# Optimization experiments

Hardware: AMD Instinct MI355X
Metric: run time of the kernel (lower is better)

The kernel has to match this reference:

```python
import jax, jax.numpy as jnp
import numpy as np

N_PTS = 100000
C_IN, C_OUT, K = 16, 32, 3
B, D, H, W = 2, 32, 128, 128


def setup_inputs() -> dict:
    key = jax.random.key(0)
    kf, kw, kb, kz, ky, kx = jax.random.split(key, 6)
    features = jax.random.normal(kf, (N_PTS, C_IN), dtype=jnp.float32)
    coords = jnp.stack([
        jax.random.randint(kb, (N_PTS,), 0, B),
        jax.random.randint(kz, (N_PTS,), 0, D),
        jax.random.randint(ky, (N_PTS,), 0, H),
        jax.random.randint(kx, (N_PTS,), 0, W),
    ], axis=1).astype(jnp.int32)
    weight = jax.random.normal(kw, (K ** 3, C_IN, C_OUT), dtype=jnp.float32) * 0.01
    bias = jnp.zeros((C_OUT,), dtype=jnp.float32)
    return {"features": features, "coords": coords, "weight": weight, "bias": bias,
            "batch_size": B, "d_sp": D, "h_sp": H, "w_sp": W}


def reference(features, coords, weight, bias, batch_size, d_sp, h_sp, w_sp):
    # Scatter sparse voxel features into dense grid (B, C_in, D, H, W).
    n, c_in = features.shape
    c_out = weight.shape[2]
    k = K
    b, z, y, x = coords[:, 0], coords[:, 1], coords[:, 2], coords[:, 3]
    dense = jnp.zeros((batch_size, c_in, d_sp, h_sp, w_sp), dtype=features.dtype)
    dense = dense.at[b, :, z, y, x].set(features)  # (N,) advanced idx -> rows of (N, C_in)
    # Conv3d: torch copies weight.view(C_out, C_in, k, k, k) -> OIDHW kernel.
    kernel = weight.reshape(c_out, c_in, k, k, k)
    out = jax.lax.conv_general_dilated(
        dense, kernel,
        window_strides=(1, 1, 1),
        padding=[(1, 1), (1, 1), (1, 1)],
        dimension_numbers=("NCDHW", "OIDHW", "NCDHW"))
    out = jax.nn.relu(out + bias[None, :, None, None, None])
    # Dense equivalent of the torch nonzero-gather (which has data-dependent
    # shape): return the full dense activated grid (B, C_out, D, H, W).
    return out
```

## Files before the change

kernel.cpp:

```cpp
#include <hip/hip_runtime.h>

#define CIN   16
#define COUT  32
#define BATCH 2
#define DSP   32
#define HSP   128
#define WSP   128
#define NVOX  (BATCH*DSP*HSP*WSP)

#define DP (DSP+2)
#define HP (HSP+2)
#define WP (WSP+2)
#define NVOXP (BATCH*DP*HP*WP)
#define NDCH  (NVOXP*2)

#define TZ 2
#define TY 4
#define TX 16
#define NTW 8
#define PZ 4
#define PYY 6
#define PXX 18
#define PROW (PYY*PXX)
#define PVOX (PZ*PROW)
#define NCHUNK (2*PVOX)
#define SLICE  (NCHUNK/4)
#define NPAIR 14
#define NWEL  (NPAIR*2*64*8)
#define NWREP ((NWEL + 255)/256)
#define NBLK  1024

typedef __bf16 bf16x8 __attribute__((ext_vector_type(8)));
typedef float  f32x4  __attribute__((ext_vector_type(4)));

__device__ __forceinline__ void load_lds16(const void* g, void* l) {
    __builtin_amdgcn_global_load_lds(
        (const __attribute__((address_space(1))) unsigned*)g,
        (__attribute__((address_space(3))) unsigned*)l, 16, 0, 0);
}

__global__ void k_prep(const int4* __restrict__ coords, int n, int nbDedup,
                       int* __restrict__ map,
                       const float* __restrict__ w, __bf16* __restrict__ wpack) {
    int bb = blockIdx.x;
    if (bb < nbDedup) {
        int p = bb * 256 + threadIdx.x;
        if (p >= n) return;
        int4 c = coords[p];
        int vox = ((c.x*DSP + c.y)*HSP + c.z)*WSP + c.w;
        atomicMax(&map[vox], p);
    } else {
        int i = (bb - nbDedup) * 256 + threadIdx.x;
        if (i >= NWEL) return;
        int j = i & 7, l = (i>>3) & 63, h = (i>>9) & 1, p = i >> 10;
        int tap = 2*p + ((l>>4)>>1);
        int co  = h*16 + (l & 15);
        int ci  = ((l>>4)&1)*8 + j;
        float v = (tap < 27) ? w[(co*CIN + ci)*27 + tap] : 0.0f;
        wpack[i] = (__bf16)v;
    }
}

__global__ void k_fill(const int* __restrict__ map, const float* __restrict__ feat,
                       __bf16* __restrict__ dense) {
    int c = blockIdx.x * 256 + threadIdx.x;
    if (c >= NDCH) return;
    int v = c >> 1, h = c & 1;
    int bb = v / (DP*HP*WP);
    int r  = v - bb*(DP*HP*WP);
    int zp = r / (HP*WP);  r -= zp*(HP*WP);
    int yp = r / WP;
    int xp = r - yp*WP;
    bf16x8 val = { (__bf16)0.f,(__bf16)0.f,(__bf16)0.f,(__bf16)0.f,
                   (__bf16)0.f,(__bf16)0.f,(__bf16)0.f,(__bf16)0.f };
    if ((unsigned)(zp-1) < DSP && (unsigned)(yp-1) < HSP && (unsigned)(xp-1) < WSP) {
        int vox = ((bb*DSP + (zp-1))*HSP + (yp-1))*WSP + (xp-1);
        int p = map[vox];
        if (p >= 0) {
            const float4* fp = (const float4*)(feat + (size_t)p*CIN) + h*2;
            float4 f0 = fp[0], f1 = fp[1];
            val = bf16x8{ (__bf16)f0.x,(__bf16)f0.y,(__bf16)f0.z,(__bf16)f0.w,
                          (__bf16)f1.x,(__bf16)f1.y,(__bf16)f1.z,(__bf16)f1.w };
        }
    }
    *(bf16x8*)(dense + (size_t)v*CIN + h*8) = val;
}

__device__ __forceinline__ void stage_tile(const __bf16* __restrict__ gb,
                                           ushort* lbase, int wave, int lane) {
    #pragma unroll
    for (int it = 0; it < 4; ++it) {
        int rel = it*64 + lane;
        if (rel < SLICE) {
            int j = wave*SLICE + rel;
            int h = (j >= PVOX) ? 1 : 0;
            int v = j - h*PVOX;
            int pz = v / PROW;
            int rm = v - pz*PROW;
            int py = rm / PXX;
            int px = rm - py*PXX;
            load_lds16(gb + ((size_t)(pz*HP*WP + py*WP + px))*CIN + h*8,
                       (void*)(lbase + (size_t)(wave*SLICE + it*64)*8));
        }
    }
}

__global__ __launch_bounds__(256, 3) void k_conv(
    const __bf16* __restrict__ dense, const __bf16* __restrict__ wpack,
    const float* __restrict__ bias, float* __restrict__ out)
{
    __shared__ __align__(16) ushort patch[2][NCHUNK*8];

    int bid = blockIdx.x;
    int bs  = (bid & 7) * (NBLK/8) + (bid >> 3);
    int tyi = bs & 31, tzi = (bs >> 5) & 15, b = bs >> 9;
    int z0 = tzi*TZ, y0 = tyi*TY;

    int tid  = threadIdx.x;
    int lane = tid & 63, wave = tid >> 6;
    int lx16  = lane & 15;
    int lhalf = (lane >> 4) & 1;
    int ltp   = (lane >> 4) >> 1;
    int lq    = lane >> 4;
    int zw    = wave >> 1;
    int yb    = (wave & 1) * 2;

    bf16x8 wf[NPAIR][2];
    #pragma unroll
    for (int p = 0; p < NPAIR; ++p)
        #pragma unroll
        for (int h = 0; h < 2; ++h)
            wf[p][h] = *(const bf16x8*)(wpack + (size_t)((p*2 + h)*64 + lane)*8);

    int voff[NPAIR];
    #pragma unroll
    for (int p = 0; p < NPAIR; ++p) {
        int tap = 2*p + ltp; if (tap > 26) tap = 26;
        int kd = tap/9, kh = (tap/3)%3, kw = tap%3;
        voff[p] = (kd*PYY + kh)*PXX + kw;
    }
    float bv0 = bias[lx16], bv1 = bias[16 + lx16];

    const __bf16* gbase = dense + ((((size_t)b*DP + z0)*HP + y0)*WP)*CIN;

    stage_tile(gbase, patch[0], wave, lane);

    #pragma unroll 1
    for (int t = 0; t < NTW; ++t) {
        if (t < NTW-1)
            stage_tile(gbase + (size_t)(t+1)*TX*CIN, patch[(t&1)^1], wave, lane);
        if (t == 0 || t == NTW-1)
            asm volatile("s_waitcnt vmcnt(4)\ns_barrier" ::: "memory");
        else
            asm volatile("s_waitcnt vmcnt(8)\ns_barrier" ::: "memory");
        __builtin_amdgcn_sched_barrier(0);

        f32x4 acc[2][2];
        acc[0][0] = (f32x4){0.f,0.f,0.f,0.f}; acc[0][1] = (f32x4){0.f,0.f,0.f,0.f};
        acc[1][0] = (f32x4){0.f,0.f,0.f,0.f}; acc[1][1] = (f32x4){0.f,0.f,0.f,0.f};
        const ushort* pb = patch[t&1] +
            ((size_t)lhalf*PVOX + (zw*PYY + yb)*PXX + lx16)*8;
        __builtin_amdgcn_s_setprio(1);
        #pragma unroll
        for (int p = 0; p < NPAIR; ++p) {
            const ushort* pa = pb + (size_t)voff[p]*8;
            #pragma unroll
            for (int gi = 0; gi < 2; ++gi) {
                bf16x8 a = *(const bf16x8*)(pa + gi*(PXX*8));
                acc[gi][0] = __builtin_amdgcn_mfma_f32_16x16x32_bf16(a, wf[p][0], acc[gi][0], 0,0,0);
                acc[gi][1] = __builtin_amdgcn_mfma_f32_16x16x32_bf16(a, wf[p][1], acc[gi][1], 0,0,0);
            }
        }
        __builtin_amdgcn_s_setprio(0);

        asm volatile("s_barrier" ::: "memory");
        __builtin_amdgcn_sched_barrier(0);

        #pragma unroll
        for (int gi = 0; gi < 2; ++gi) {
            int gz = z0 + zw, gy = y0 + yb + gi;
            int gx = t*TX + (lq << 2);
            f32x4 o0, o1;
            o0[0] = fmaxf(acc[gi][0][0]+bv0, 0.f); o0[1] = fmaxf(acc[gi][0][1]+bv0, 0.f);
            o0[2] = fmaxf(acc[gi][0][2]+bv0, 0.f); o0[3] = fmaxf(acc[gi][0][3]+bv0, 0.f);
            o1[0] = fmaxf(acc[gi][1][0]+bv1, 0.f); o1[1] = fmaxf(acc[gi][1][1]+bv1, 0.f);
            o1[2] = fmaxf(acc[gi][1][2]+bv1, 0.f); o1[3] = fmaxf(acc[gi][1][3]+bv1, 0.f);
            size_t base0 = ((((size_t)b*COUT + lx16)*DSP + gz)*HSP + gy)*WSP + gx;
            size_t base1 = base0 + (size_t)16*DSP*HSP*WSP;
            *(f32x4*)(out + base0) = o0;
            *(f32x4*)(out + base1) = o1;
        }
    }
}

extern "C" void kernel_launch(void* const* d_in, const int* in_sizes, int n_in,
                              void* d_out, int out_size, void* d_ws, size_t ws_size,
                              hipStream_t stream) {
    const float* feat   = (const float*)d_in[0];
    const int4*  coords = (const int4*)d_in[1];
    const float* weight = (const float*)d_in[2];
    const float* bias   = (const float*)d_in[3];
    float* out = (float*)d_out;
    int n = in_sizes[0] / CIN;

    int*    map   = (int*)d_ws;
    __bf16* dense = (__bf16*)(map + NVOX);
    __bf16* wpack = dense + (size_t)NVOXP*CIN;

    (void)hipMemsetAsync(map, 0xFF, (size_t)NVOX*sizeof(int), stream);

    int nb = (n + 255) / 256;
    k_prep<<<nb + NWREP, 256, 0, stream>>>(coords, n, nb, map, weight, wpack);
    k_fill<<<(NDCH + 255)/256, 256, 0, stream>>>(map, feat, dense);
    k_conv<<<NBLK, 256, 0, stream>>>(dense, wpack, bias, out);
}
```

Before: 69.54 us.

## Switch conv to 32x32x16 MFMA with per-tap K=16 and wider x tiles

Replaces the 16x16x32 MFMA scheme, which packed two taps per instruction and padded the 27 taps to 28, with 32x32x16 MFMAs. Each instruction now covers one tap with all 16 input channels and all 32 output channels, so the padded wasted tap goes away and operand handling is simpler. The block tile is reshaped to 2x2x32 voxels with a 4x4x34 patch, which doubles the block count and halves the x-windows per block. The staging and wait counts are adjusted to match. The trade-off is a 27-long dependent accumulator chain per wave with less independent MFMA work to hide latency, plus a changed halo overhead ratio.

```diff
diff --git a/kernel.cpp b/kernel.cpp
--- a/kernel.cpp
+++ b/kernel.cpp
@@ -15,23 +15,24 @@
 #define NDCH  (NVOXP*2)
 
 #define TZ 2
-#define TY 4
-#define TX 16
-#define NTW 8
+#define TY 2
+#define TX 32
+#define NTW 4
 #define PZ 4
-#define PYY 6
-#define PXX 18
+#define PYY 4
+#define PXX 34
 #define PROW (PYY*PXX)
 #define PVOX (PZ*PROW)
+#define HALFCH PVOX
 #define NCHUNK (2*PVOX)
 #define SLICE  (NCHUNK/4)
-#define NPAIR 14
-#define NWEL  (NPAIR*2*64*8)
+#define NWEL  (27*64*8)
 #define NWREP ((NWEL + 255)/256)
-#define NBLK  1024
+#define NBLK  2048
 
 typedef __bf16 bf16x8 __attribute__((ext_vector_type(8)));
 typedef float  f32x4  __attribute__((ext_vector_type(4)));
+typedef float  f32x16 __attribute__((ext_vector_type(16)));
 
 __device__ __forceinline__ void load_lds16(const void* g, void* l) {
     __builtin_amdgcn_global_load_lds(
@@ -52,12 +53,10 @@
     } else {
         int i = (bb - nbDedup) * 256 + threadIdx.x;
         if (i >= NWEL) return;
-        int j = i & 7, l = (i>>3) & 63, h = (i>>9) & 1, p = i >> 10;
-        int tap = 2*p + ((l>>4)>>1);
-        int co  = h*16 + (l & 15);
-        int ci  = ((l>>4)&1)*8 + j;
-        float v = (tap < 27) ? w[(co*CIN + ci)*27 + tap] : 0.0f;
-        wpack[i] = (__bf16)v;
+        int j = i & 7, l = (i>>3) & 63, tap = i >> 9;
+        int co = l & 31;
+        int ci = (l >> 5)*8 + j;
+        wpack[i] = (__bf16)w[(co*CIN + ci)*27 + tap];
     }
 }
 
@@ -89,7 +88,7 @@
 __device__ __forceinline__ void stage_tile(const __bf16* __restrict__ gb,
                                            ushort* lbase, int wave, int lane) {
     #pragma unroll
-    for (int it = 0; it < 4; ++it) {
+    for (int it = 0; it < 5; ++it) {
         int rel = it*64 + lane;
         if (rel < SLICE) {
             int j = wave*SLICE + rel;
@@ -113,33 +112,22 @@
 
     int bid = blockIdx.x;
     int bs  = (bid & 7) * (NBLK/8) + (bid >> 3);
-    int tyi = bs & 31, tzi = (bs >> 5) & 15, b = bs >> 9;
+    int tyi = bs & 63, tzi = (bs >> 6) & 15, b = bs >> 10;
     int z0 = tzi*TZ, y0 = tyi*TY;
 
     int tid  = threadIdx.x;
     int lane = tid & 63, wave = tid >> 6;
-    int lx16  = lane & 15;
-    int lhalf = (lane >> 4) & 1;
-    int ltp   = (lane >> 4) >> 1;
-    int lq    = lane >> 4;
-    int zw    = wave >> 1;
-    int yb    = (wave & 1) * 2;
+    int cout = lane & 31;
+    int hi   = lane >> 5;
+    int zl   = wave >> 1;
+    int yl   = wave & 1;
 
-    bf16x8 wf[NPAIR][2];
+    bf16x8 wf[27];
     #pragma unroll
-    for (int p = 0; p < NPAIR; ++p)
-        #pragma unroll
-        for (int h = 0; h < 2; ++h)
-            wf[p][h] = *(const bf16x8*)(wpack + (size_t)((p*2 + h)*64 + lane)*8);
+    for (int tap = 0; tap < 27; ++tap)
+        wf[tap] = *(const bf16x8*)(wpack + (size_t)(tap*64 + lane)*8);
 
-    int voff[NPAIR];
-    #pragma unroll
-    for (int p = 0; p < NPAIR; ++p) {
-        int tap = 2*p + ltp; if (tap > 26) tap = 26;
-        int kd = tap/9, kh = (tap/3)%3, kw = tap%3;
-        voff[p] = (kd*PYY + kh)*PXX + kw;
-    }
-    float bv0 = bias[lx16], bv1 = bias[16 + lx16];
+    float bv = bias[cout];
 
     const __bf16* gbase = dense + ((((size_t)b*DP + z0)*HP + y0)*WP)*CIN;
 
@@ -149,46 +137,41 @@
     for (int t = 0; t < NTW; ++t) {
         if (t < NTW-1)
             stage_tile(gbase + (size_t)(t+1)*TX*CIN, patch[(t&1)^1], wave, lane);
-        if (t == 0 || t == NTW-1)
-            asm volatile("s_waitcnt vmcnt(4)\ns_barrier" ::: "memory");
-        else
-            asm volatile("s_waitcnt vmcnt(8)\ns_barrier" ::: "memory");
+        if (t == 0)          asm volatile("s_waitcnt vmcnt(5)\ns_barrier" ::: "memory");
+        else if (t < NTW-1)  asm volatile("s_waitcnt vmcnt(9)\ns_barrier" ::: "memory");
+        else                 asm volatile("s_waitcnt vmcnt(4)\ns_barrier" ::: "memory");
         __builtin_amdgcn_sched_barrier(0);
 
-        f32x4 acc[2][2];
-        acc[0][0] = (f32x4){0.f,0.f,0.f,0.f}; acc[0][1] = (f32x4){0.f,0.f,0.f,0.f};
-        acc[1][0] = (f32x4){0.f,0.f,0.f,0.f}; acc[1][1] = (f32x4){0.f,0.f,0.f,0.f};
-        const ushort* pb = patch[t&1] +
-            ((size_t)lhalf*PVOX + (zw*PYY + yb)*PXX + lx16)*8;
+        f32x16 acc = {0.f,0.f,0.f,0.f,0.f,0.f,0.f,0.f,
+                      0.f,0.f,0.f,0.f,0.f,0.f,0.f,0.f};
+        const ushort* pbase = patch[t&1] +
+            ((size_t)hi*HALFCH + (zl*PYY + yl)*PXX + (lane & 31))*8;
         __builtin_amdgcn_s_setprio(1);
         #pragma unroll
-        for (int p = 0; p < NPAIR; ++p) {
-            const ushort* pa = pb + (size_t)voff[p]*8;
-            #pragma unroll
-            for (int gi = 0; gi < 2; ++gi) {
-                bf16x8 a = *(const bf16x8*)(pa + gi*(PXX*8));
-                acc[gi][0] = __builtin_amdgcn_mfma_f32_16x16x32_bf16(a, wf[p][0], acc[gi][0], 0,0,0);
-                acc[gi][1] = __builtin_amdgcn_mfma_f32_16x16x32_bf16(a, wf[p][1], acc[gi][1], 0,0,0);
-            }
+        for (int kd = 0; kd < 3; ++kd)
+        #pragma unroll
+        for (int kh = 0; kh < 3; ++kh)
+        #pragma unroll
+        for (int kw = 0; kw < 3; ++kw) {
+            int tap = (kd*3 + kh)*3 + kw;
+            bf16x8 a = *(const bf16x8*)(pbase + ((kd*PYY + kh)*PXX + kw)*8);
+            acc = __builtin_amdgcn_mfma_f32_32x32x16_bf16(a, wf[tap], acc, 0, 0, 0);
         }
         __builtin_amdgcn_s_setprio(0);
 
         asm volatile("s_barrier" ::: "memory");
         __builtin_amdgcn_sched_barrier(0);
 
+        int gz = z0 + zl, gy = y0 + yl;
+        size_t rowbase = ((((size_t)b*COUT + cout)*DSP + gz)*HSP + gy)*WSP + t*TX;
         #pragma unroll
-        for (int gi = 0; gi < 2; ++gi) {
-            int gz = z0 + zw, gy = y0 + yb + gi;
-            int gx = t*TX + (lq << 2);
-            f32x4 o0, o1;
-            o0[0] = fmaxf(acc[gi][0][0]+bv0, 0.f); o0[1] = fmaxf(acc[gi][0][1]+bv0, 0.f);
-            o0[2] = fmaxf(acc[gi][0][2]+bv0, 0.f); o0[3] = fmaxf(acc[gi][0][3]+bv0, 0.f);
-            o1[0] = fmaxf(acc[gi][1][0]+bv1, 0.f); o1[1] = fmaxf(acc[gi][1][1]+bv1, 0.f);
-            o1[2] = fmaxf(acc[gi][1][2]+bv1, 0.f); o1[3] = fmaxf(acc[gi][1][3]+bv1, 0.f);
-            size_t base0 = ((((size_t)b*COUT + lx16)*DSP + gz)*HSP + gy)*WSP + gx;
-            size_t base1 = base0 + (size_t)16*DSP*HSP*WSP;
-            *(f32x4*)(out + base0) = o0;
-            *(f32x4*)(out + base1) = o1;
+        for (int q = 0; q < 4; ++q) {
+            f32x4 o;
+            o[0] = fmaxf(acc[q*4+0] + bv, 0.f);
+            o[1] = fmaxf(acc[q*4+1] + bv, 0.f);
+            o[2] = fmaxf(acc[q*4+2] + bv, 0.f);
+            o[3] = fmaxf(acc[q*4+3] + bv, 0.f);
+            *(f32x4*)(out + rowbase + q*8 + hi*4) = o;
         }
     }
 }
```

Result: slower. 73.14 us (+5.2%).
